# Kernel tuning notes

Hardware: AMD Instinct MI355X
Metric: run time of the kernel (lower is better)

Reference implementation:

```python
import jax, jax.numpy as jnp
import numpy as np

N = 50000
E = 800000
IN_CH = 128
HID = 32
HEADS = 8
OUT_CH = 64
NEG_SLOPE = 0.2  # PyG GATConv default leaky_relu slope


def setup_inputs() -> dict:
    key = jax.random.key(0)
    ks = jax.random.split(key, 16)
    x = jax.random.normal(ks[0], (N, IN_CH), dtype=jnp.float32)
    edge_index = jax.random.randint(ks[1], (2, E), 0, N, dtype=jnp.int64)
    s = 0.1
    return {
        "x": x,
        "edge_index": edge_index,
        # layer 1: in -> (HEADS, HID), concat
        "W1": jax.random.normal(ks[2], (IN_CH, HEADS * HID), dtype=jnp.float32) * s,
        "att_src1": jax.random.normal(ks[3], (HEADS, HID), dtype=jnp.float32) * s,
        "att_dst1": jax.random.normal(ks[4], (HEADS, HID), dtype=jnp.float32) * s,
        "b1": jnp.zeros((HEADS * HID,), dtype=jnp.float32),
        # layer 2: HEADS*HID -> (HEADS, HID), concat
        "W2": jax.random.normal(ks[5], (HEADS * HID, HEADS * HID), dtype=jnp.float32) * s,
        "att_src2": jax.random.normal(ks[6], (HEADS, HID), dtype=jnp.float32) * s,
        "att_dst2": jax.random.normal(ks[7], (HEADS, HID), dtype=jnp.float32) * s,
        "b2": jnp.zeros((HEADS * HID,), dtype=jnp.float32),
        # layer 3: HEADS*HID -> (1, OUT_CH), no concat (heads=1)
        "W3": jax.random.normal(ks[8], (HEADS * HID, OUT_CH), dtype=jnp.float32) * s,
        "att_src3": jax.random.normal(ks[9], (1, OUT_CH), dtype=jnp.float32) * s,
        "att_dst3": jax.random.normal(ks[10], (1, OUT_CH), dtype=jnp.float32) * s,
        "b3": jnp.zeros((OUT_CH,), dtype=jnp.float32),
    }


def gat_conv(x, src, dst, W, a_src, a_dst, b, heads, ch, concat):
    n = x.shape[0]
    h = (x @ W).reshape(n, heads, ch)                      # [N,H,C]
    alpha_src = jnp.sum(h * a_src, axis=-1)                # [N,H]
    alpha_dst = jnp.sum(h * a_dst, axis=-1)                # [N,H]
    logits = jax.nn.leaky_relu(alpha_src[src] + alpha_dst[dst], NEG_SLOPE)  # [E,H]
    # numerically stable softmax over edges grouped by destination node
    m = jax.ops.segment_max(logits, dst, num_segments=n)   # [N,H]
    m = jnp.where(jnp.isfinite(m), m, 0.0)
    e = jnp.exp(logits - m[dst])                           # [E,H]
    denom = jax.ops.segment_sum(e, dst, num_segments=n)    # [N,H]
    alpha = e / (denom[dst] + 1e-16)                       # [E,H]
    # weighted scatter-aggregate of source features
    out = jax.ops.segment_sum(alpha[:, :, None] * h[src], dst, num_segments=n)  # [N,H,C]
    out = out.reshape(n, heads * ch) if concat else out.mean(axis=1)
    return out + b


def reference(x, edge_index, W1, att_src1, att_dst1, b1,
              W2, att_src2, att_dst2, b2, W3, att_src3, att_dst3, b3):
    src, dst = edge_index[0], edge_index[1]
    h = jax.nn.elu(gat_conv(x, src, dst, W1, att_src1, att_dst1, b1, HEADS, HID, True))
    h = jax.nn.elu(gat_conv(h, src, dst, W2, att_src2, att_dst2, b2, HEADS, HID, True))
    out = gat_conv(h, src, dst, W3, att_src3, att_dst3, b3, 1, OUT_CH, False)
    return out
```

## Files before the change

kernel.cpp:

```cpp
#include <hip/hip_runtime.h>
#include <hip/hip_bf16.h>
#include <hip/hip_fp16.h>
#include <stdint.h>

#define NNODES 50000
#define NEDGES 800000
#define LOG2E 1.44269504088896340736f

typedef float f32x4 __attribute__((ext_vector_type(4)));
typedef _Float16 half8 __attribute__((ext_vector_type(8)));
typedef _Float16 half2v __attribute__((ext_vector_type(2)));
typedef unsigned short ushort8v __attribute__((ext_vector_type(8)));

__device__ __forceinline__ ushort f2h(float f) {
  return __half_as_ushort(__float2half(f));
}
__device__ __forceinline__ float2 h2x2(uint32_t u) {
  return __half22float2(__builtin_bit_cast(__half2, u));
}

#if __has_builtin(__builtin_amdgcn_fdot2) && __has_builtin(__builtin_amdgcn_perm) && __has_builtin(__builtin_amdgcn_cvt_pkrtz)
#define USE_DOT2 1
#else
#define USE_DOT2 0
#endif

__device__ __forceinline__ half2v pack2(float a, float b) {
  return __builtin_bit_cast(half2v, __builtin_amdgcn_cvt_pkrtz(a, b));
}

__device__ __forceinline__ float fexp2(float x) {
#if __has_builtin(__builtin_amdgcn_exp2f)
  return __builtin_amdgcn_exp2f(x);
#else
  return exp2f(x);
#endif
}

__device__ __forceinline__ void gload_lds16(const void* g, void* l) {
  __builtin_amdgcn_global_load_lds(
      (const __attribute__((address_space(1))) uint32_t*)g,
      (__attribute__((address_space(3))) uint32_t*)l, 16, 0, 0);
}

__global__ __launch_bounds__(256) void gemm_wide(
    const ushort* __restrict__ A, const ushort* __restrict__ B,
    const float* __restrict__ a_src, const float* __restrict__ a_dst,
    float* __restrict__ as_out, float* __restrict__ ad_out,
    ushort* __restrict__ Cout, int M, int K) {
  __shared__ ushort As[64 * 64];
  __shared__ ushort Bs[256 * 64];

  const int t = threadIdx.x;
  const int w = t >> 6, ln = t & 63;
  const int row0 = blockIdx.x * 64;
  const int wr = (w >> 1) * 32, wc = (w & 1) * 128;

  f32x4 acc[2][8] = {};

  const int nkt = K >> 6;
  for (int kt = 0; kt < nkt; ++kt) {
    const int k0 = kt << 6;
    #pragma unroll
    for (int i = 0; i < 2; ++i) {
      int row8 = w * 2 + i;
      int rloc = row8 * 8 + (ln >> 3);
      int slot = (ln & 7) ^ (rloc & 7);
      int grow = row0 + rloc; grow = grow < M ? grow : M - 1;
      gload_lds16(A + (size_t)grow * K + k0 + slot * 8, As + row8 * 512);
    }
    #pragma unroll
    for (int i = 0; i < 8; ++i) {
      int row8 = w * 8 + i;
      int rloc = row8 * 8 + (ln >> 3);
      int slot = (ln & 7) ^ (rloc & 7);
      gload_lds16(B + (size_t)rloc * K + k0 + slot * 8, Bs + row8 * 512);
    }
    __syncthreads();

    #pragma unroll
    for (int ks = 0; ks < 2; ++ks) {
      half8 a[2], b[8];
      #pragma unroll
      for (int i = 0; i < 2; ++i) {
        int row = wr + i * 16 + (ln & 15);
        int slot = (ks * 4 + (ln >> 4)) ^ (row & 7);
        a[i] = *(const half8*)(As + row * 64 + slot * 8);
      }
      #pragma unroll
      for (int j = 0; j < 8; ++j) {
        int col = wc + j * 16 + (ln & 15);
        int slot = (ks * 4 + (ln >> 4)) ^ (col & 7);
        b[j] = *(const half8*)(Bs + col * 64 + slot * 8);
      }
      #pragma unroll
      for (int i = 0; i < 2; ++i)
        #pragma unroll
        for (int j = 0; j < 8; ++j)
          acc[i][j] = __builtin_amdgcn_mfma_f32_16x16x32_f16(a[i], b[j], acc[i][j], 0, 0, 0);
    }
    __syncthreads();
  }

  const int lx = ln & 15, g = ln >> 4;

  #pragma unroll
  for (int i = 0; i < 2; ++i)
    #pragma unroll
    for (int j = 0; j < 8; ++j)
      #pragma unroll
      for (int r = 0; r < 4; ++r) {
        int grow = row0 + wr + i * 16 + g * 4 + r;
        int gcol = wc + j * 16 + lx;
        if (grow < M) Cout[(size_t)grow * 256 + gcol] = f2h(acc[i][j][r]);
      }

  const int hbase = wc >> 5;
  float avs[8], avd[8];
  #pragma unroll
  for (int j = 0; j < 8; ++j) {
    avs[j] = a_src[wc + j * 16 + lx] * LOG2E;
    avd[j] = a_dst[wc + j * 16 + lx] * LOG2E;
  }
  #pragma unroll
  for (int i = 0; i < 2; ++i)
    #pragma unroll
    for (int r = 0; r < 4; ++r) {
      float ps[4] = {0.f, 0.f, 0.f, 0.f}, pd[4] = {0.f, 0.f, 0.f, 0.f};
      #pragma unroll
      for (int j = 0; j < 8; ++j) {
        float v = acc[i][j][r];
        ps[j >> 1] += v * avs[j];
        pd[j >> 1] += v * avd[j];
      }
      #pragma unroll
      for (int m = 1; m < 16; m <<= 1)
        #pragma unroll
        for (int q = 0; q < 4; ++q) {
          ps[q] += __shfl_xor(ps[q], m);
          pd[q] += __shfl_xor(pd[q], m);
        }
      if (lx == 0) {
        int grow = row0 + wr + i * 16 + g * 4 + r;
        if (grow < M) {
          #pragma unroll
          for (int q = 0; q < 4; ++q) {
            as_out[grow * 8 + hbase + q] = ps[q];
            ad_out[grow * 8 + hbase + q] = pd[q];
          }
        }
      }
    }
}

__global__ __launch_bounds__(256) void gemm_mfma3(
    const ushort* __restrict__ A, const ushort* __restrict__ B,
    const float* __restrict__ a_src, const float* __restrict__ a_dst,
    float* __restrict__ as_out, float* __restrict__ ad_out,
    ushort* __restrict__ Cout, int M, int K, int Ncols) {
  __shared__ ushort As[128 * 64];
  __shared__ ushort Bs[64 * 64];
  __shared__ float redS[2][128], redD[2][128];

  const int t = threadIdx.x;
  const int w = t >> 6, ln = t & 63;
  const int row0 = blockIdx.y * 128;
  const int col0 = blockIdx.x * 64;
  const int wr = (w >> 1) * 64, wc = (w & 1) * 32;

  f32x4 acc[4][2] = {};

  const int nkt = K >> 6;
  for (int kt = 0; kt < nkt; ++kt) {
    const int k0 = kt << 6;
    #pragma unroll
    for (int i = 0; i < 4; ++i) {
      int row8 = w * 4 + i;
      int rloc = row8 * 8 + (ln >> 3);
      int slot = (ln & 7) ^ (rloc & 7);
      int grow = row0 + rloc; grow = grow < M ? grow : M - 1;
      gload_lds16(A + (size_t)grow * K + k0 + slot * 8, As + row8 * 512);
    }
    #pragma unroll
    for (int i = 0; i < 2; ++i) {
      int row8 = w * 2 + i;
      int rloc = row8 * 8 + (ln >> 3);
      int slot = (ln & 7) ^ (rloc & 7);
      gload_lds16(B + (size_t)(col0 + rloc) * K + k0 + slot * 8, Bs + row8 * 512);
    }
    __syncthreads();

    #pragma unroll
    for (int ks = 0; ks < 2; ++ks) {
      half8 a[4], b[2];
      #pragma unroll
      for (int i = 0; i < 4; ++i) {
        int row = wr + i * 16 + (ln & 15);
        int slot = (ks * 4 + (ln >> 4)) ^ (row & 7);
        a[i] = *(const half8*)(As + row * 64 + slot * 8);
      }
      #pragma unroll
      for (int j = 0; j < 2; ++j) {
        int col = wc + j * 16 + (ln & 15);
        int slot = (ks * 4 + (ln >> 4)) ^ (col & 7);
        b[j] = *(const half8*)(Bs + col * 64 + slot * 8);
      }
      #pragma unroll
      for (int i = 0; i < 4; ++i)
        #pragma unroll
        for (int j = 0; j < 2; ++j)
          acc[i][j] = __builtin_amdgcn_mfma_f32_16x16x32_f16(a[i], b[j], acc[i][j], 0, 0, 0);
    }
    __syncthreads();
  }

  const int lx = ln & 15, g = ln >> 4;

  #pragma unroll
  for (int i = 0; i < 4; ++i)
    #pragma unroll
    for (int j = 0; j < 2; ++j)
      #pragma unroll
      for (int r = 0; r < 4; ++r) {
        int grow = row0 + wr + i * 16 + g * 4 + r;
        int gcol = col0 + wc + j * 16 + lx;
        if (grow < M) Cout[(size_t)grow * Ncols + gcol] = f2h(acc[i][j][r]);
      }

  float avs[2], avd[2];
  #pragma unroll
  for (int j = 0; j < 2; ++j) {
    avs[j] = a_src[wc + j * 16 + lx] * LOG2E;
    avd[j] = a_dst[wc + j * 16 + lx] * LOG2E;
  }
  #pragma unroll
  for (int i = 0; i < 4; ++i)
    #pragma unroll
    for (int r = 0; r < 4; ++r) {
      float ps = 0.f, pd = 0.f;
      #pragma unroll
      for (int j = 0; j < 2; ++j) {
        float v = acc[i][j][r];
        ps += v * avs[j];
        pd += v * avd[j];
      }
      #pragma unroll
      for (int m = 1; m < 16; m <<= 1) {
        ps += __shfl_xor(ps, m);
        pd += __shfl_xor(pd, m);
      }
      if (lx == 0) {
        int lrow = wr + i * 16 + g * 4 + r;
        redS[w & 1][lrow] = ps;
        redD[w & 1][lrow] = pd;
      }
    }
  __syncthreads();
  if (t < 128) {
    int grow = row0 + t;
    if (grow < M) {
      as_out[grow] = redS[0][t] + redS[1][t];
      ad_out[grow] = redD[0][t] + redD[1][t];
    }
  }
}

__global__ void cvt_h(const float* __restrict__ in, ushort* __restrict__ out, int n4) {
  int idx = blockIdx.x * blockDim.x + threadIdx.x;
  if (idx >= n4) return;
  float4 v = ((const float4*)in)[idx];
  ushort4 o;
  o.x = f2h(v.x); o.y = f2h(v.y); o.z = f2h(v.z); o.w = f2h(v.w);
  ((ushort4*)out)[idx] = o;
}

__global__ void cvt_w_all(const float* __restrict__ W1, const float* __restrict__ W2,
                          const float* __restrict__ W3, ushort* __restrict__ w1t,
                          ushort* __restrict__ w2t, ushort* __restrict__ w3t) {
  int idx = blockIdx.x * blockDim.x + threadIdx.x;
  if (idx < 32768) {
    int k = idx >> 8, c = idx & 255;
    w1t[(size_t)c * 128 + k] = f2h(W1[idx]);
  } else if (idx < 32768 + 65536) {
    int j = idx - 32768;
    int k = j >> 8, c = j & 255;
    w2t[(size_t)c * 256 + k] = f2h(W2[j]);
  } else if (idx < 32768 + 65536 + 16384) {
    int j = idx - 98304;
    int k = j >> 6, c = j & 63;
    w3t[(size_t)c * 256 + k] = f2h(W3[j]);
  }
}

__global__ void deg_kernel(const int* __restrict__ dst, int* __restrict__ deg, int E) {
  int e = blockIdx.x * blockDim.x + threadIdx.x;
  if (e < E) atomicAdd(&deg[dst[e]], 1);
}

__global__ __launch_bounds__(256) void scan_partial(const int* __restrict__ deg,
                                                    int* __restrict__ rowptr,
                                                    int* __restrict__ blocksum, int n) {
  __shared__ int sdata[256];
  int t = threadIdx.x;
  int base = blockIdx.x * 1024 + t * 4;
  int v[4], s = 0;
  #pragma unroll
  for (int i = 0; i < 4; ++i) {
    v[i] = (base + i < n) ? deg[base + i] : 0;
    s += v[i];
  }
  sdata[t] = s;
  __syncthreads();
  for (int off = 1; off < 256; off <<= 1) {
    int x = (t >= off) ? sdata[t - off] : 0;
    __syncthreads();
    sdata[t] += x;
    __syncthreads();
  }
  int run = sdata[t] - s;
  #pragma unroll
  for (int i = 0; i < 4; ++i) {
    if (base + i < n) rowptr[base + i] = run;
    run += v[i];
  }
  if (t == 255) blocksum[blockIdx.x] = sdata[255];
}

__global__ __launch_bounds__(256) void scan_blocksums(int* __restrict__ blocksum, int nb) {
  __shared__ int sdata[256];
  int t = threadIdx.x;
  int v = (t < nb) ? blocksum[t] : 0;
  sdata[t] = v;
  __syncthreads();
  for (int off = 1; off < 256; off <<= 1) {
    int x = (t >= off) ? sdata[t - off] : 0;
    __syncthreads();
    sdata[t] += x;
    __syncthreads();
  }
  if (t < nb) blocksum[t] = sdata[t] - v;
}

__global__ void scan_add(int* __restrict__ rowptr, const int* __restrict__ blocksum,
                         int* __restrict__ cursor, int n, int E) {
  int idx = blockIdx.x * blockDim.x + threadIdx.x;
  if (idx < n) {
    rowptr[idx] += blocksum[idx >> 10];
    cursor[idx] = 0;
  }
  if (idx == n) rowptr[n] = E;
}

__global__ void scatter_kernel(const int* __restrict__ src, const int* __restrict__ dst,
                               const int* __restrict__ rowptr, int* __restrict__ cursor,
                               int* __restrict__ col_src, int E) {
  int e = blockIdx.x * blockDim.x + threadIdx.x;
  if (e >= E) return;
  int d = dst[e];
  int pos = rowptr[d] + atomicAdd(&cursor[d], 1);
  col_src[pos] = src[e];
}

__global__ __launch_bounds__(256) void aggr_h(
    const int* __restrict__ rowptr, const int* __restrict__ col_src,
    const ushort* __restrict__ h, const float* __restrict__ as_,
    const float* __restrict__ ad_, const float* __restrict__ bias,
    ushort* __restrict__ of, int n) {
  int d = blockIdx.x * 4 + (threadIdx.x >> 6);
  if (d >= n) return;
  int lane = threadIdx.x & 63;
  int half = lane >> 5;
  int l = lane & 31;
  int c0 = l * 8;
  int hd = l >> 2;
  float ad_d = ad_[d * 8 + hd];
  float a0 = 0.f, a1 = 0.f, a2 = 0.f, a3 = 0.f;
  float a4 = 0.f, a5 = 0.f, a6 = 0.f, a7 = 0.f, denom = 0.f;
  const ushort* hp = h + c0;
  int beg = rowptr[d], end = rowptr[d + 1];
  int i = beg + half;
#if USE_DOT2
  for (; i + 6 < end; i += 8) {
    int s0 = col_src[i],     s1 = col_src[i + 2];
    int s2 = col_src[i + 4], s3 = col_src[i + 6];
    float l0 = as_[s0 * 8 + hd] + ad_d;
    float l1 = as_[s1 * 8 + hd] + ad_d;
    float l2 = as_[s2 * 8 + hd] + ad_d;
    float l3 = as_[s3 * 8 + hd] + ad_d;
    uint4 v0 = *(const uint4*)(hp + (size_t)s0 * 256);
    uint4 v1 = *(const uint4*)(hp + (size_t)s1 * 256);
    uint4 v2 = *(const uint4*)(hp + (size_t)s2 * 256);
    uint4 v3 = *(const uint4*)(hp + (size_t)s3 * 256);
    float e0 = fexp2(fmaxf(l0, 0.2f * l0));
    float e1 = fexp2(fmaxf(l1, 0.2f * l1));
    float e2 = fexp2(fmaxf(l2, 0.2f * l2));
    float e3 = fexp2(fmaxf(l3, 0.2f * l3));
    denom += (e0 + e1) + (e2 + e3);
    half2v ep01 = pack2(e0, e1);
    half2v ep23 = pack2(e2, e3);
    uint32_t p;
    p = __builtin_amdgcn_perm(v1.x, v0.x, 0x05040100u);
    a0 = __builtin_amdgcn_fdot2(ep01, __builtin_bit_cast(half2v, p), a0, false);
    p = __builtin_amdgcn_perm(v1.x, v0.x, 0x07060302u);
    a1 = __builtin_amdgcn_fdot2(ep01, __builtin_bit_cast(half2v, p), a1, false);
    p = __builtin_amdgcn_perm(v1.y, v0.y, 0x05040100u);
    a2 = __builtin_amdgcn_fdot2(ep01, __builtin_bit_cast(half2v, p), a2, false);
    p = __builtin_amdgcn_perm(v1.y, v0.y, 0x07060302u);
    a3 = __builtin_amdgcn_fdot2(ep01, __builtin_bit_cast(half2v, p), a3, false);
    p = __builtin_amdgcn_perm(v1.z, v0.z, 0x05040100u);
    a4 = __builtin_amdgcn_fdot2(ep01, __builtin_bit_cast(half2v, p), a4, false);
    p = __builtin_amdgcn_perm(v1.z, v0.z, 0x07060302u);
    a5 = __builtin_amdgcn_fdot2(ep01, __builtin_bit_cast(half2v, p), a5, false);
    p = __builtin_amdgcn_perm(v1.w, v0.w, 0x05040100u);
    a6 = __builtin_amdgcn_fdot2(ep01, __builtin_bit_cast(half2v, p), a6, false);
    p = __builtin_amdgcn_perm(v1.w, v0.w, 0x07060302u);
    a7 = __builtin_amdgcn_fdot2(ep01, __builtin_bit_cast(half2v, p), a7, false);
    p = __builtin_amdgcn_perm(v3.x, v2.x, 0x05040100u);
    a0 = __builtin_amdgcn_fdot2(ep23, __builtin_bit_cast(half2v, p), a0, false);
    p = __builtin_amdgcn_perm(v3.x, v2.x, 0x07060302u);
    a1 = __builtin_amdgcn_fdot2(ep23, __builtin_bit_cast(half2v, p), a1, false);
    p = __builtin_amdgcn_perm(v3.y, v2.y, 0x05040100u);
    a2 = __builtin_amdgcn_fdot2(ep23, __builtin_bit_cast(half2v, p), a2, false);
    p = __builtin_amdgcn_perm(v3.y, v2.y, 0x07060302u);
    a3 = __builtin_amdgcn_fdot2(ep23, __builtin_bit_cast(half2v, p), a3, false);
    p = __builtin_amdgcn_perm(v3.z, v2.z, 0x05040100u);
    a4 = __builtin_amdgcn_fdot2(ep23, __builtin_bit_cast(half2v, p), a4, false);
    p = __builtin_amdgcn_perm(v3.z, v2.z, 0x07060302u);
    a5 = __builtin_amdgcn_fdot2(ep23, __builtin_bit_cast(half2v, p), a5, false);
    p = __builtin_amdgcn_perm(v3.w, v2.w, 0x05040100u);
    a6 = __builtin_amdgcn_fdot2(ep23, __builtin_bit_cast(half2v, p), a6, false);
    p = __builtin_amdgcn_perm(v3.w, v2.w, 0x07060302u);
    a7 = __builtin_amdgcn_fdot2(ep23, __builtin_bit_cast(half2v, p), a7, false);
  }
  for (; i + 2 < end; i += 4) {
    int s0 = col_src[i], s1 = col_src[i + 2];
    float l0 = as_[s0 * 8 + hd] + ad_d;
    float l1 = as_[s1 * 8 + hd] + ad_d;
    uint4 v0 = *(const uint4*)(hp + (size_t)s0 * 256);
    uint4 v1 = *(const uint4*)(hp + (size_t)s1 * 256);
    float e0 = fexp2(fmaxf(l0, 0.2f * l0));
    float e1 = fexp2(fmaxf(l1, 0.2f * l1));
    denom += e0 + e1;
    half2v ep = pack2(e0, e1);
    uint32_t p;
    p = __builtin_amdgcn_perm(v1.x, v0.x, 0x05040100u);
    a0 = __builtin_amdgcn_fdot2(ep, __builtin_bit_cast(half2v, p), a0, false);
    p = __builtin_amdgcn_perm(v1.x, v0.x, 0x07060302u);
    a1 = __builtin_amdgcn_fdot2(ep, __builtin_bit_cast(half2v, p), a1, false);
    p = __builtin_amdgcn_perm(v1.y, v0.y, 0x05040100u);
    a2 = __builtin_amdgcn_fdot2(ep, __builtin_bit_cast(half2v, p), a2, false);
    p = __builtin_amdgcn_perm(v1.y, v0.y, 0x07060302u);
    a3 = __builtin_amdgcn_fdot2(ep, __builtin_bit_cast(half2v, p), a3, false);
    p = __builtin_amdgcn_perm(v1.z, v0.z, 0x05040100u);
    a4 = __builtin_amdgcn_fdot2(ep, __builtin_bit_cast(half2v, p), a4, false);
    p = __builtin_amdgcn_perm(v1.z, v0.z, 0x07060302u);
    a5 = __builtin_amdgcn_fdot2(ep, __builtin_bit_cast(half2v, p), a5, false);
    p = __builtin_amdgcn_perm(v1.w, v0.w, 0x05040100u);
    a6 = __builtin_amdgcn_fdot2(ep, __builtin_bit_cast(half2v, p), a6, false);
    p = __builtin_amdgcn_perm(v1.w, v0.w, 0x07060302u);
    a7 = __builtin_amdgcn_fdot2(ep, __builtin_bit_cast(half2v, p), a7, false);
  }
#endif
  for (; i < end; i += 2) {
    int s = col_src[i];
    float lg = as_[s * 8 + hd] + ad_d;
    float ev = fexp2(fmaxf(lg, 0.2f * lg));
    denom += ev;
    uint4 v = *(const uint4*)(hp + (size_t)s * 256);
    float2 p0 = h2x2(v.x), p1 = h2x2(v.y), p2 = h2x2(v.z), p3 = h2x2(v.w);
    a0 += ev * p0.x; a1 += ev * p0.y;
    a2 += ev * p1.x; a3 += ev * p1.y;
    a4 += ev * p2.x; a5 += ev * p2.y;
    a6 += ev * p3.x; a7 += ev * p3.y;
  }
  a0 += __shfl_xor(a0, 32); a1 += __shfl_xor(a1, 32);
  a2 += __shfl_xor(a2, 32); a3 += __shfl_xor(a3, 32);
  a4 += __shfl_xor(a4, 32); a5 += __shfl_xor(a5, 32);
  a6 += __shfl_xor(a6, 32); a7 += __shfl_xor(a7, 32);
  denom += __shfl_xor(denom, 32);
  if (half == 0) {
    float inv = 1.f / (denom + 1e-16f);
    float4 b0 = *(const float4*)(bias + c0);
    float4 b1 = *(const float4*)(bias + c0 + 4);
    float vv[8];
    vv[0] = a0 * inv + b0.x; vv[1] = a1 * inv + b0.y;
    vv[2] = a2 * inv + b0.z; vv[3] = a3 * inv + b0.w;
    vv[4] = a4 * inv + b1.x; vv[5] = a5 * inv + b1.y;
    vv[6] = a6 * inv + b1.z; vv[7] = a7 * inv + b1.w;
    ushort8v hh;
    #pragma unroll
    for (int j = 0; j < 8; ++j) {
      float v = vv[j];
      v = (v > 0.f) ? v : expm1f(v);
      hh[j] = f2h(v);
    }
    *(ushort8v*)(of + (size_t)d * 256 + c0) = hh;
  }
}

__global__ __launch_bounds__(256) void aggr_f3(
    const int* __restrict__ rowptr, const int* __restrict__ col_src,
    const ushort* __restrict__ h, const float* __restrict__ as_,
    const float* __restrict__ ad_, const float* __restrict__ bias,
    float* __restrict__ outp, int n) {
  int wid = (blockIdx.x * 256 + threadIdx.x) >> 6;
  int d = wid * 4 + ((threadIdx.x >> 4) & 3);
  if (d >= n) return;
  int l = threadIdx.x & 15;
  int c0 = l * 4;
  float ad_d = ad_[d];
  float a0 = 0.f, a1 = 0.f, a2 = 0.f, a3 = 0.f, denom = 0.f;
  const ushort* hp = h + c0;
  int beg = rowptr[d], end = rowptr[d + 1];
  int i = beg;
#if USE_DOT2
  const half2v onepk = {(_Float16)1.f, (_Float16)1.f};
  for (; i + 2 <= end; i += 2) {
    int s0 = col_src[i], s1 = col_src[i + 1];
    float l0 = as_[s0] + ad_d;
    float l1 = as_[s1] + ad_d;
    uint2 v0 = *(const uint2*)(hp + (size_t)s0 * 64);
    uint2 v1 = *(const uint2*)(hp + (size_t)s1 * 64);
    float e0 = fexp2(fmaxf(l0, 0.2f * l0));
    float e1 = fexp2(fmaxf(l1, 0.2f * l1));
    half2v ep = pack2(e0, e1);
    denom = __builtin_amdgcn_fdot2(ep, onepk, denom, false);
    uint32_t p;
    p = __builtin_amdgcn_perm(v1.x, v0.x, 0x05040100u);
    a0 = __builtin_amdgcn_fdot2(ep, __builtin_bit_cast(half2v, p), a0, false);
    p = __builtin_amdgcn_perm(v1.x, v0.x, 0x07060302u);
    a1 = __builtin_amdgcn_fdot2(ep, __builtin_bit_cast(half2v, p), a1, false);
    p = __builtin_amdgcn_perm(v1.y, v0.y, 0x05040100u);
    a2 = __builtin_amdgcn_fdot2(ep, __builtin_bit_cast(half2v, p), a2, false);
    p = __builtin_amdgcn_perm(v1.y, v0.y, 0x07060302u);
    a3 = __builtin_amdgcn_fdot2(ep, __builtin_bit_cast(half2v, p), a3, false);
  }
#endif
  for (; i < end; ++i) {
    int s = col_src[i];
    float lg = as_[s] + ad_d;
    float ev = fexp2(fmaxf(lg, 0.2f * lg));
    denom += ev;
    uint2 v = *(const uint2*)(hp + (size_t)s * 64);
    float2 p0 = h2x2(v.x), p1 = h2x2(v.y);
    a0 += ev * p0.x;
    a1 += ev * p0.y;
    a2 += ev * p1.x;
    a3 += ev * p1.y;
  }
  float inv = 1.f / (denom + 1e-16f);
  float4 r;
  r.x = a0 * inv + bias[c0 + 0];
  r.y = a1 * inv + bias[c0 + 1];
  r.z = a2 * inv + bias[c0 + 2];
  r.w = a3 * inv + bias[c0 + 3];
  *(float4*)(outp + (size_t)d * 64 + c0) = r;
}


extern "C" void kernel_launch(void* const* d_in, const int* in_sizes, int n_in,
                              void* d_out, int out_size, void* d_ws, size_t ws_size,
                              hipStream_t stream) {
  const float* x   = (const float*)d_in[0];
  const int*   ei  = (const int*)d_in[1];
  const float* W1  = (const float*)d_in[2];
  const float* aS1 = (const float*)d_in[3];
  const float* aD1 = (const float*)d_in[4];
  const float* b1  = (const float*)d_in[5];
  const float* W2  = (const float*)d_in[6];
  const float* aS2 = (const float*)d_in[7];
  const float* aD2 = (const float*)d_in[8];
  const float* b2  = (const float*)d_in[9];
  const float* W3  = (const float*)d_in[10];
  const float* aS3 = (const float*)d_in[11];
  const float* aD3 = (const float*)d_in[12];
  const float* b3  = (const float*)d_in[13];

  const int* srcp = ei;
  const int* dstp = ei + NEDGES;

  char* base = (char*)d_ws;
  size_t o = 0;
  ushort* hbf  = (ushort*)(base + o); o += 25600000;
  ushort* ff   = (ushort*)(base + o); o += 25600000;
  ushort* f1   = (ushort*)(base + o); o += 12800000;
  float*  as_  = (float*)(base + o);  o += 1600000;
  float*  ad_  = (float*)(base + o);  o += 1600000;
  ushort* w1t  = (ushort*)(base + o); o += 65536;
  ushort* w2t  = (ushort*)(base + o); o += 131072;
  ushort* w3t  = (ushort*)(base + o); o += 32768;
  int* rowptr  = (int*)(base + o);    o += 200016;
  int* cursor  = (int*)(base + o);    o += 200000;
  int* colsrc  = (int*)(base + o);    o += 3200000;
  int* bsum    = (int*)(base + o);    o += 1024;
  float* outp  = (float*)d_out;

  hipMemsetAsync(cursor, 0, NNODES * sizeof(int), stream);
  deg_kernel<<<(NEDGES + 255) / 256, 256, 0, stream>>>(dstp, cursor, NEDGES);
  int nb = (NNODES + 1023) / 1024;
  scan_partial<<<nb, 256, 0, stream>>>(cursor, rowptr, bsum, NNODES);
  scan_blocksums<<<1, 256, 0, stream>>>(bsum, nb);
  scan_add<<<(NNODES + 256) / 256, 256, 0, stream>>>(rowptr, bsum, cursor, NNODES, NEDGES);
  scatter_kernel<<<(NEDGES + 255) / 256, 256, 0, stream>>>(srcp, dstp, rowptr, cursor,
                                                           colsrc, NEDGES);

  cvt_h<<<(NNODES * 128 / 4 + 255) / 256, 256, 0, stream>>>(x, f1, NNODES * 128 / 4);
  cvt_w_all<<<(114688 + 255) / 256, 256, 0, stream>>>(W1, W2, W3, w1t, w2t, w3t);

  const int ga  = (NNODES + 3) / 4;
  const int ga4 = (NNODES + 15) / 16;
  const int gw  = (NNODES + 63) / 64;
  gemm_wide<<<gw, 256, 0, stream>>>(f1, w1t, aS1, aD1, as_, ad_, hbf, NNODES, 128);
  aggr_h<<<ga, 256, 0, stream>>>(rowptr, colsrc, hbf, as_, ad_, b1, ff, NNODES);
  gemm_wide<<<gw, 256, 0, stream>>>(ff, w2t, aS2, aD2, as_, ad_, hbf, NNODES, 256);
  aggr_h<<<ga, 256, 0, stream>>>(rowptr, colsrc, hbf, as_, ad_, b2, ff, NNODES);
  gemm_mfma3<<<dim3(1, (NNODES + 127) / 128), 256, 0, stream>>>(
      ff, w3t, aS3, aD3, as_, ad_, hbf, NNODES, 256, 64);
  aggr_f3<<<ga4, 256, 0, stream>>>(rowptr, colsrc, hbf, as_, ad_, b3, outp, NNODES);
}
```

Before: 324.1 us.

## Fuse fp32 input conversion into GEMM, merge prep kernels, rework layer-3 aggregation

The first GEMM now loads fp32 x directly into LDS and converts to fp16 while reading fragments, which removes the separate cvt_h pass and its intermediate buffer. The degree count and weight transposes are merged into one prep kernel. The block-sum scan is folded into scan_add by serially prefix-summing the block sums per block. The layer-3 aggregation changes from 16 lanes per node to a full wave per node, with 8 edge groups reduced by shuffles, to get more memory-level parallelism on high-degree nodes. The costs are a doubled LDS A tile and in-loop conversion work in the first GEMM, and a redundant serial scan in every scan_add block.

```diff
diff --git a/kernel.cpp b/kernel.cpp
--- a/kernel.cpp
+++ b/kernel.cpp
@@ -43,12 +43,14 @@
       (__attribute__((address_space(3))) uint32_t*)l, 16, 0, 0);
 }
 
+template <int AF32>
 __global__ __launch_bounds__(256) void gemm_wide(
-    const ushort* __restrict__ A, const ushort* __restrict__ B,
+    const ushort* __restrict__ A, const float* __restrict__ Af,
+    const ushort* __restrict__ B,
     const float* __restrict__ a_src, const float* __restrict__ a_dst,
     float* __restrict__ as_out, float* __restrict__ ad_out,
     ushort* __restrict__ Cout, int M, int K) {
-  __shared__ ushort As[64 * 64];
+  __shared__ ushort As[AF32 ? 8192 : 4096];
   __shared__ ushort Bs[256 * 64];
 
   const int t = threadIdx.x;
@@ -61,13 +63,25 @@
   const int nkt = K >> 6;
   for (int kt = 0; kt < nkt; ++kt) {
     const int k0 = kt << 6;
-    #pragma unroll
-    for (int i = 0; i < 2; ++i) {
-      int row8 = w * 2 + i;
-      int rloc = row8 * 8 + (ln >> 3);
-      int slot = (ln & 7) ^ (rloc & 7);
-      int grow = row0 + rloc; grow = grow < M ? grow : M - 1;
-      gload_lds16(A + (size_t)grow * K + k0 + slot * 8, As + row8 * 512);
+    if constexpr (AF32) {
+      #pragma unroll
+      for (int i = 0; i < 4; ++i) {
+        int row4 = w * 4 + i;
+        int rloc = row4 * 4 + (ln >> 4);
+        int sl = ln & 15;
+        int sg = sl ^ ((rloc & 7) << 1);
+        int grow = row0 + rloc; grow = grow < M ? grow : M - 1;
+        gload_lds16(Af + (size_t)grow * K + k0 + sg * 4, As + row4 * 512);
+      }
+    } else {
+      #pragma unroll
+      for (int i = 0; i < 2; ++i) {
+        int row8 = w * 2 + i;
+        int rloc = row8 * 8 + (ln >> 3);
+        int slot = (ln & 7) ^ (rloc & 7);
+        int grow = row0 + rloc; grow = grow < M ? grow : M - 1;
+        gload_lds16(A + (size_t)grow * K + k0 + slot * 8, As + row8 * 512);
+      }
     }
     #pragma unroll
     for (int i = 0; i < 8; ++i) {
@@ -84,8 +98,21 @@
       #pragma unroll
       for (int i = 0; i < 2; ++i) {
         int row = wr + i * 16 + (ln & 15);
-        int slot = (ks * 4 + (ln >> 4)) ^ (row & 7);
-        a[i] = *(const half8*)(As + row * 64 + slot * 8);
+        if constexpr (AF32) {
+          int ch = (ks * 4 + (ln >> 4)) ^ (row & 7);
+          const float* rp = (const float*)As + row * 64 + ch * 8;
+          f32x4 f0 = *(const f32x4*)rp;
+          f32x4 f1 = *(const f32x4*)(rp + 4);
+          union { half8 h; uint32_t u[4]; } cv;
+          cv.u[0] = __builtin_bit_cast(uint32_t, pack2(f0[0], f0[1]));
+          cv.u[1] = __builtin_bit_cast(uint32_t, pack2(f0[2], f0[3]));
+          cv.u[2] = __builtin_bit_cast(uint32_t, pack2(f1[0], f1[1]));
+          cv.u[3] = __builtin_bit_cast(uint32_t, pack2(f1[2], f1[3]));
+          a[i] = cv.h;
+        } else {
+          int slot = (ks * 4 + (ln >> 4)) ^ (row & 7);
+          a[i] = *(const half8*)(As + row * 64 + slot * 8);
+        }
       }
       #pragma unroll
       for (int j = 0; j < 8; ++j) {
@@ -265,36 +292,28 @@
   }
 }
 
-__global__ void cvt_h(const float* __restrict__ in, ushort* __restrict__ out, int n4) {
+__global__ void prep_kernel(const int* __restrict__ dst, int* __restrict__ deg,
+                            const float* __restrict__ W1, const float* __restrict__ W2,
+                            const float* __restrict__ W3, ushort* __restrict__ w1t,
+                            ushort* __restrict__ w2t, ushort* __restrict__ w3t) {
   int idx = blockIdx.x * blockDim.x + threadIdx.x;
-  if (idx >= n4) return;
-  float4 v = ((const float4*)in)[idx];
-  ushort4 o;
-  o.x = f2h(v.x); o.y = f2h(v.y); o.z = f2h(v.z); o.w = f2h(v.w);
-  ((ushort4*)out)[idx] = o;
-}
-
-__global__ void cvt_w_all(const float* __restrict__ W1, const float* __restrict__ W2,
-                          const float* __restrict__ W3, ushort* __restrict__ w1t,
-                          ushort* __restrict__ w2t, ushort* __restrict__ w3t) {
-  int idx = blockIdx.x * blockDim.x + threadIdx.x;
-  if (idx < 32768) {
-    int k = idx >> 8, c = idx & 255;
-    w1t[(size_t)c * 128 + k] = f2h(W1[idx]);
-  } else if (idx < 32768 + 65536) {
-    int j = idx - 32768;
+  if (idx < NEDGES) {
+    atomicAdd(&deg[dst[idx]], 1);
+    return;
+  }
+  int j = idx - NEDGES;
+  if (j < 32768) {
     int k = j >> 8, c = j & 255;
-    w2t[(size_t)c * 256 + k] = f2h(W2[j]);
-  } else if (idx < 32768 + 65536 + 16384) {
-    int j = idx - 98304;
-    int k = j >> 6, c = j & 63;
-    w3t[(size_t)c * 256 + k] = f2h(W3[j]);
-  }
-}
-
-__global__ void deg_kernel(const int* __restrict__ dst, int* __restrict__ deg, int E) {
-  int e = blockIdx.x * blockDim.x + threadIdx.x;
-  if (e < E) atomicAdd(&deg[dst[e]], 1);
+    w1t[(size_t)c * 128 + k] = f2h(W1[j]);
+  } else if (j < 32768 + 65536) {
+    int q = j - 32768;
+    int k = q >> 8, c = q & 255;
+    w2t[(size_t)c * 256 + k] = f2h(W2[q]);
+  } else if (j < 32768 + 65536 + 16384) {
+    int q = j - 98304;
+    int k = q >> 6, c = q & 63;
+    w3t[(size_t)c * 256 + k] = f2h(W3[q]);
+  }
 }
 
 __global__ __launch_bounds__(256) void scan_partial(const int* __restrict__ deg,
@@ -326,26 +345,18 @@
   if (t == 255) blocksum[blockIdx.x] = sdata[255];
 }
 
-__global__ __launch_bounds__(256) void scan_blocksums(int* __restrict__ blocksum, int nb) {
-  __shared__ int sdata[256];
+__global__ void scan_add(int* __restrict__ rowptr, const int* __restrict__ blocksum,
+                         int* __restrict__ cursor, int n, int E, int nb) {
+  __shared__ int soff[64];
   int t = threadIdx.x;
-  int v = (t < nb) ? blocksum[t] : 0;
-  sdata[t] = v;
+  if (t == 0) {
+    int run = 0;
+    for (int i = 0; i < nb; ++i) { soff[i] = run; run += blocksum[i]; }
+  }
   __syncthreads();
-  for (int off = 1; off < 256; off <<= 1) {
-    int x = (t >= off) ? sdata[t - off] : 0;
-    __syncthreads();
-    sdata[t] += x;
-    __syncthreads();
-  }
-  if (t < nb) blocksum[t] = sdata[t] - v;
-}
-
-__global__ void scan_add(int* __restrict__ rowptr, const int* __restrict__ blocksum,
-                         int* __restrict__ cursor, int n, int E) {
-  int idx = blockIdx.x * blockDim.x + threadIdx.x;
+  int idx = blockIdx.x * blockDim.x + t;
   if (idx < n) {
-    rowptr[idx] += blocksum[idx >> 10];
+    rowptr[idx] += soff[idx >> 10];
     cursor[idx] = 0;
   }
   if (idx == n) rowptr[n] = E;
@@ -503,58 +514,49 @@
     const ushort* __restrict__ h, const float* __restrict__ as_,
     const float* __restrict__ ad_, const float* __restrict__ bias,
     float* __restrict__ outp, int n) {
-  int wid = (blockIdx.x * 256 + threadIdx.x) >> 6;
-  int d = wid * 4 + ((threadIdx.x >> 4) & 3);
+  int d = blockIdx.x * 4 + (threadIdx.x >> 6);
   if (d >= n) return;
-  int l = threadIdx.x & 15;
-  int c0 = l * 4;
+  int lane = threadIdx.x & 63;
+  int g = lane >> 3;
+  int l = lane & 7;
+  int c0 = l * 8;
   float ad_d = ad_[d];
-  float a0 = 0.f, a1 = 0.f, a2 = 0.f, a3 = 0.f, denom = 0.f;
+  float a0 = 0.f, a1 = 0.f, a2 = 0.f, a3 = 0.f;
+  float a4 = 0.f, a5 = 0.f, a6 = 0.f, a7 = 0.f, denom = 0.f;
   const ushort* hp = h + c0;
   int beg = rowptr[d], end = rowptr[d + 1];
-  int i = beg;
-#if USE_DOT2
-  const half2v onepk = {(_Float16)1.f, (_Float16)1.f};
-  for (; i + 2 <= end; i += 2) {
-    int s0 = col_src[i], s1 = col_src[i + 1];
-    float l0 = as_[s0] + ad_d;
-    float l1 = as_[s1] + ad_d;
-    uint2 v0 = *(const uint2*)(hp + (size_t)s0 * 64);
-    uint2 v1 = *(const uint2*)(hp + (size_t)s1 * 64);
-    float e0 = fexp2(fmaxf(l0, 0.2f * l0));
-    float e1 = fexp2(fmaxf(l1, 0.2f * l1));
-    half2v ep = pack2(e0, e1);
-    denom = __builtin_amdgcn_fdot2(ep, onepk, denom, false);
-    uint32_t p;
-    p = __builtin_amdgcn_perm(v1.x, v0.x, 0x05040100u);
-    a0 = __builtin_amdgcn_fdot2(ep, __builtin_bit_cast(half2v, p), a0, false);
-    p = __builtin_amdgcn_perm(v1.x, v0.x, 0x07060302u);
-    a1 = __builtin_amdgcn_fdot2(ep, __builtin_bit_cast(half2v, p), a1, false);
-    p = __builtin_amdgcn_perm(v1.y, v0.y, 0x05040100u);
-    a2 = __builtin_amdgcn_fdot2(ep, __builtin_bit_cast(half2v, p), a2, false);
-    p = __builtin_amdgcn_perm(v1.y, v0.y, 0x07060302u);
-    a3 = __builtin_amdgcn_fdot2(ep, __builtin_bit_cast(half2v, p), a3, false);
-  }
-#endif
-  for (; i < end; ++i) {
+  for (int i = beg + g; i < end; i += 8) {
     int s = col_src[i];
     float lg = as_[s] + ad_d;
     float ev = fexp2(fmaxf(lg, 0.2f * lg));
     denom += ev;
-    uint2 v = *(const uint2*)(hp + (size_t)s * 64);
-    float2 p0 = h2x2(v.x), p1 = h2x2(v.y);
-    a0 += ev * p0.x;
-    a1 += ev * p0.y;
-    a2 += ev * p1.x;
-    a3 += ev * p1.y;
-  }
-  float inv = 1.f / (denom + 1e-16f);
-  float4 r;
-  r.x = a0 * inv + bias[c0 + 0];
-  r.y = a1 * inv + bias[c0 + 1];
-  r.z = a2 * inv + bias[c0 + 2];
-  r.w = a3 * inv + bias[c0 + 3];
-  *(float4*)(outp + (size_t)d * 64 + c0) = r;
+    uint4 v = *(const uint4*)(hp + (size_t)s * 64);
+    float2 p0 = h2x2(v.x), p1 = h2x2(v.y), p2 = h2x2(v.z), p3 = h2x2(v.w);
+    a0 += ev * p0.x; a1 += ev * p0.y;
+    a2 += ev * p1.x; a3 += ev * p1.y;
+    a4 += ev * p2.x; a5 += ev * p2.y;
+    a6 += ev * p3.x; a7 += ev * p3.y;
+  }
+  #pragma unroll
+  for (int m = 8; m < 64; m <<= 1) {
+    a0 += __shfl_xor(a0, m); a1 += __shfl_xor(a1, m);
+    a2 += __shfl_xor(a2, m); a3 += __shfl_xor(a3, m);
+    a4 += __shfl_xor(a4, m); a5 += __shfl_xor(a5, m);
+    a6 += __shfl_xor(a6, m); a7 += __shfl_xor(a7, m);
+    denom += __shfl_xor(denom, m);
+  }
+  if (g == 0) {
+    float inv = 1.f / (denom + 1e-16f);
+    float4 b0 = *(const float4*)(bias + c0);
+    float4 b1 = *(const float4*)(bias + c0 + 4);
+    float4 r0, r1;
+    r0.x = a0 * inv + b0.x; r0.y = a1 * inv + b0.y;
+    r0.z = a2 * inv + b0.z; r0.w = a3 * inv + b0.w;
+    r1.x = a4 * inv + b1.x; r1.y = a5 * inv + b1.y;
+    r1.z = a6 * inv + b1.z; r1.w = a7 * inv + b1.w;
+    *(float4*)(outp + (size_t)d * 64 + c0) = r0;
+    *(float4*)(outp + (size_t)d * 64 + c0 + 4) = r1;
+  }
 }
 
 
@@ -583,7 +585,6 @@
   size_t o = 0;
   ushort* hbf  = (ushort*)(base + o); o += 25600000;
   ushort* ff   = (ushort*)(base + o); o += 25600000;
-  ushort* f1   = (ushort*)(base + o); o += 12800000;
   float*  as_  = (float*)(base + o);  o += 1600000;
   float*  ad_  = (float*)(base + o);  o += 1600000;
   ushort* w1t  = (ushort*)(base + o); o += 65536;
@@ -596,25 +597,24 @@
   float* outp  = (float*)d_out;
 
   hipMemsetAsync(cursor, 0, NNODES * sizeof(int), stream);
-  deg_kernel<<<(NEDGES + 255) / 256, 256, 0, stream>>>(dstp, cursor, NEDGES);
+  prep_kernel<<<(NEDGES + 114688 + 255) / 256, 256, 0, stream>>>(
+      dstp, cursor, W1, W2, W3, w1t, w2t, w3t);
   int nb = (NNODES + 1023) / 1024;
   scan_partial<<<nb, 256, 0, stream>>>(cursor, rowptr, bsum, NNODES);
-  scan_blocksums<<<1, 256, 0, stream>>>(bsum, nb);
-  scan_add<<<(NNODES + 256) / 256, 256, 0, stream>>>(rowptr, bsum, cursor, NNODES, NEDGES);
+  scan_add<<<(NNODES + 256) / 256, 256, 0, stream>>>(rowptr, bsum, cursor, NNODES,
+                                                     NEDGES, nb);
   scatter_kernel<<<(NEDGES + 255) / 256, 256, 0, stream>>>(srcp, dstp, rowptr, cursor,
                                                            colsrc, NEDGES);
 
-  cvt_h<<<(NNODES * 128 / 4 + 255) / 256, 256, 0, stream>>>(x, f1, NNODES * 128 / 4);
-  cvt_w_all<<<(114688 + 255) / 256, 256, 0, stream>>>(W1, W2, W3, w1t, w2t, w3t);
-
-  const int ga  = (NNODES + 3) / 4;
-  const int ga4 = (NNODES + 15) / 16;
-  const int gw  = (NNODES + 63) / 64;
-  gemm_wide<<<gw, 256, 0, stream>>>(f1, w1t, aS1, aD1, as_, ad_, hbf, NNODES, 128);
+  const int ga = (NNODES + 3) / 4;
+  const int gw = (NNODES + 63) / 64;
+  gemm_wide<1><<<gw, 256, 0, stream>>>(nullptr, x, w1t, aS1, aD1, as_, ad_,
+                                       hbf, NNODES, 128);
   aggr_h<<<ga, 256, 0, stream>>>(rowptr, colsrc, hbf, as_, ad_, b1, ff, NNODES);
-  gemm_wide<<<gw, 256, 0, stream>>>(ff, w2t, aS2, aD2, as_, ad_, hbf, NNODES, 256);
+  gemm_wide<0><<<gw, 256, 0, stream>>>(ff, nullptr, w2t, aS2, aD2, as_, ad_,
+                                       hbf, NNODES, 256);
   aggr_h<<<ga, 256, 0, stream>>>(rowptr, colsrc, hbf, as_, ad_, b2, ff, NNODES);
   gemm_mfma3<<<dim3(1, (NNODES + 127) / 128), 256, 0, stream>>>(
       ff, w3t, aS3, aD3, as_, ad_, hbf, NNODES, 256, 64);
-  aggr_f3<<<ga4, 256, 0, stream>>>(rowptr, colsrc, hbf, as_, ad_, b3, outp, NNODES);
-}
+  aggr_f3<<<ga, 256, 0, stream>>>(rowptr, colsrc, hbf, as_, ad_, b3, outp, NNODES);
+}
```

After: 314.5 us. 3.0% less time.
